# Kernel optimization log

Hardware: AMD Instinct MI355X
Metric: run time of the kernel (lower is better)

The kernel has to match this reference:

```python
import jax, jax.numpy as jnp
import numpy as np


def setup_inputs() -> dict:
    key = jax.random.key(0)
    k1, k2, k3 = jax.random.split(key, 3)
    B, H, S, D = 2, 16, 2048, 64
    return {
        "q": jax.random.normal(k1, (B, H, S, D), dtype=jnp.float32),
        "k": jax.random.normal(k2, (B, H, S, D), dtype=jnp.float32),
        "v": jax.random.normal(k3, (B, H, S, D), dtype=jnp.float32),
        "chunk_size": 256,
    }


def reference(q, k, v, chunk_size):
    # Chunked Based linear attention: linear (K^T V) + rank-3 quadratic (K x K x V)
    # inter-chunk state recurrence (shifted/exclusive cumsum over chunks) plus the
    # intra-chunk causal part with kernel  s = q.k;  phi = s + 0.5*s^2.
    B, H, S, D = q.shape
    C = chunk_size
    N = S // C
    scale = D ** (-0.5)

    qc = (q * scale).reshape(B, H, N, C, D)
    kc = k.reshape(B, H, N, C, D)
    vc = v.reshape(B, H, N, C, D)

    # ---- linear inter-chunk state: shifted cumsum of K^T V per chunk ----
    KV = jnp.einsum("bhncd,bhnce->bhnde", kc, vc)            # (B,H,N,D,D)
    S_lin = jnp.cumsum(KV, axis=2) - KV                       # exclusive cumsum
    o_lin = jnp.einsum("bhncd,bhnde->bhnce", qc, S_lin)

    # ---- quadratic inter-chunk state: shifted cumsum of sum_c K_d K_e V_f ----
    KKV = jnp.einsum("bhncd,bhnce,bhncf->bhndef", kc, kc, vc)  # (B,H,N,D,D,D)
    S_quad = jnp.cumsum(KKV, axis=2) - KKV                     # exclusive cumsum
    o_quad = 0.5 * jnp.einsum("bhndef,bhncd,bhnce->bhncf", S_quad, qc, qc)

    # ---- intra-chunk causal quadratic attention ----
    A = jnp.einsum("bhncd,bhnmd->bhncm", qc, kc)               # (B,H,N,C,C)
    mask = jnp.tril(jnp.ones((C, C), dtype=bool))
    Ak = jnp.where(mask, A + 0.5 * A * A, 0.0)
    o_intra = jnp.einsum("bhncm,bhnmf->bhncf", Ak, vc)

    out = (o_lin + o_quad + o_intra).reshape(B, H, S, D)
    return out
```

## Files before the change

kernel.cpp:

```cpp
#include <hip/hip_runtime.h>
#include <stdint.h>

#define SEQ  2048
#define DH   64
#define BH_N 32
#define SCALE 0.125f

typedef __attribute__((ext_vector_type(8))) short short8;
typedef __attribute__((ext_vector_type(4))) short short4b;
typedef __attribute__((ext_vector_type(4))) float f32x4;

static __device__ __forceinline__ unsigned short f2bf(float f) {
  unsigned int u = __float_as_uint(f);
  u += 0x7fffu + ((u >> 16) & 1u);
  return (unsigned short)(u >> 16);
}
static __device__ __forceinline__ unsigned packbf(float a, float b) {
  unsigned ua = __float_as_uint(a); ua += 0x7fffu + ((ua >> 16) & 1u);
  unsigned ub = __float_as_uint(b); ub += 0x7fffu + ((ub >> 16) & 1u);
  return __builtin_amdgcn_perm(ub, ua, 0x07060302);
}

typedef __attribute__((address_space(1))) const unsigned char* gp1;
typedef __attribute__((address_space(3))) unsigned char* lp3;
static __device__ __forceinline__ void stage16(const void* g, void* l) {
  __builtin_amdgcn_global_load_lds((gp1)g, (lp3)l, 16, 0, 0);
}

__global__ __launch_bounds__(256) void prep_kernel(
    const float* __restrict__ kin, const float* __restrict__ vin,
    unsigned short* __restrict__ kb2, unsigned short* __restrict__ vt2)
{
  const int sb = blockIdx.x;
  const int bh = blockIdx.y;
  const int t  = threadIdx.x;
  __shared__ __align__(16) unsigned short lds[4096];
  const size_t base  = ((size_t)bh * SEQ + (size_t)sb * 64) * DH;
  const size_t obase = ((size_t)bh * 32 + sb) * 4096;

  #pragma unroll
  for (int i = 0; i < 4; ++i) {
    int idx = i * 256 + t, key = idx >> 4, F = (idx & 15) * 4;
    float4 f = *reinterpret_cast<const float4*>(kin + base + key * DH + F);
    int c = (F >> 5) * 4 + ((F >> 3) & 3), jh = (F >> 2) & 1;
    uint2 pk; pk.x = packbf(f.x, f.y); pk.y = packbf(f.z, f.w);
    *reinterpret_cast<uint2*>(lds + (c * 64 + key) * 8 + jh * 4) = pk;
  }
  __syncthreads();
  #pragma unroll
  for (int uu = 0; uu < 2; ++uu) {
    int u = uu * 256 + t;
    *reinterpret_cast<uint4*>(kb2 + obase + u * 8) =
        *reinterpret_cast<const uint4*>(lds + u * 8);
  }
  __syncthreads();
  #pragma unroll
  for (int i = 0; i < 4; ++i) {
    int idx = i * 256 + t, key = idx >> 4, F = (idx & 15) * 4;
    float4 f = *reinterpret_cast<const float4*>(vin + base + key * DH + F);
    int kgp = key >> 5, qd = (key >> 2) & 3, jj = ((key >> 4) & 1) * 4 + (key & 3);
    int u0 = kgp * 256 + (F >> 4) * 64 + qd * 16 + (F & 15);
    lds[(u0 + 0) * 8 + jj] = f2bf(f.x);
    lds[(u0 + 1) * 8 + jj] = f2bf(f.y);
    lds[(u0 + 2) * 8 + jj] = f2bf(f.z);
    lds[(u0 + 3) * 8 + jj] = f2bf(f.w);
  }
  __syncthreads();
  #pragma unroll
  for (int uu = 0; uu < 2; ++uu) {
    int u = uu * 256 + t;
    *reinterpret_cast<uint4*>(vt2 + obase + u * 8) =
        *reinterpret_cast<const uint4*>(lds + u * 8);
  }
}

__global__ __launch_bounds__(256, 2) void attn_kernel(
    const float* __restrict__ q,
    const unsigned short* __restrict__ kb2,
    const unsigned short* __restrict__ vt2,
    float* __restrict__ out)
{
  const int qa   = blockIdx.x;
  const int bh   = blockIdx.y;
  const int tid  = threadIdx.x;
  const int w    = tid >> 6;
  const int lane = tid & 63;
  const int low  = lane & 15;
  const int quad = lane >> 4;
  const int p    = w >> 1;
  const int rh   = w & 1;
  const int nB   = 32 - qa;

  __shared__ __align__(16) unsigned short kls[2][2][4096];
  __shared__ __align__(16) unsigned short vls[2][2][4096];

  const unsigned short* kb_h = kb2 + (size_t)bh * 32 * 4096;
  const unsigned short* v2_h = vt2 + (size_t)bh * 32 * 4096;

  short8 aqA[2][2], aqB[2][2];
  #pragma unroll
  for (int tsel = 0; tsel < 2; ++tsel) {
    const int qt = tsel ? (31 - qa) : qa;
    #pragma unroll
    for (int h = 0; h < 2; ++h) {
      const float* qp =
          q + ((size_t)bh * SEQ + qt * 64 + rh * 32 + h * 16 + low) * DH + quad * 8;
      #pragma unroll
      for (int ks = 0; ks < 2; ++ks) {
        float4 f0 = *reinterpret_cast<const float4*>(qp + ks * 32);
        float4 f1 = *reinterpret_cast<const float4*>(qp + ks * 32 + 4);
        uint4 uv;
        uv.x = packbf(f0.x * SCALE, f0.y * SCALE);
        uv.y = packbf(f0.z * SCALE, f0.w * SCALE);
        uv.z = packbf(f1.x * SCALE, f1.y * SCALE);
        uv.w = packbf(f1.z * SCALE, f1.w * SCALE);
        short8 a = __builtin_bit_cast(short8, uv);
        if (tsel) aqB[h][ks] = a; else aqA[h][ks] = a;
      }
    }
  }

  f32x4 oaccA[2][4], oaccB[2][4];
  #pragma unroll
  for (int h = 0; h < 2; ++h)
    #pragma unroll
    for (int i = 0; i < 4; ++i) {
      oaccA[h][i] = (f32x4){0.f, 0.f, 0.f, 0.f};
      oaccB[h][i] = (f32x4){0.f, 0.f, 0.f, 0.f};
    }

  const int slot = w & 1;
  const unsigned short* gsrc = (w >> 1) ? v2_h : kb_h;
  unsigned short* ldst0 = (w >> 1) ? &vls[0][slot][0] : &kls[0][slot][0];
  unsigned short* ldst1 = (w >> 1) ? &vls[1][slot][0] : &kls[1][slot][0];

  #define STAGE(I, B)                                                          \
    do {                                                                       \
      int s_ = 2 * (I) + slot; if (s_ > 32) s_ = 32;                           \
      const int T_ = (s_ < nB) ? s_ : (s_ - nB);                               \
      const unsigned short* gs_ = gsrc + (size_t)T_ * 4096;                    \
      unsigned short* ld_ = (B) ? ldst1 : ldst0;                               \
      _Pragma("unroll")                                                        \
      for (int r_ = 0; r_ < 8; ++r_)                                           \
        stage16(gs_ + (r_ * 64 + lane) * 8, ld_ + (r_ * 64 + lane) * 8);       \
    } while (0)

  #define COMPUTE(AQ, OACC)                                                    \
    do {                                                                       \
      _Pragma("unroll")                                                        \
      for (int ntp = 0; ntp < 2; ++ntp) {                                      \
        short8 vf[4];                                                          \
        _Pragma("unroll")                                                      \
        for (int ft = 0; ft < 4; ++ft)                                         \
          vf[ft] = *reinterpret_cast<const short8*>(                           \
              vT + ((ntp * 4 + ft) * 64 + quad * 16 + low) * 8);               \
        _Pragma("unroll")                                                      \
        for (int sub = 0; sub < 2; ++sub) {                                    \
          const int nt = ntp * 2 + sub;                                        \
          f32x4 s0 = (f32x4){0.f, 0.f, 0.f, 0.f};                              \
          f32x4 s1 = (f32x4){0.f, 0.f, 0.f, 0.f};                              \
          _Pragma("unroll")                                                    \
          for (int ks = 0; ks < 2; ++ks) {                                     \
            short8 kf = *reinterpret_cast<const short8*>(                      \
                kT + ((ks * 4 + quad) * 64 + nt * 16 + low) * 8);              \
            s0 = __builtin_amdgcn_mfma_f32_16x16x32_bf16(kf, AQ[0][ks], s0, 0, 0, 0); \
            s1 = __builtin_amdgcn_mfma_f32_16x16x32_bf16(kf, AQ[1][ks], s1, 0, 0, 0); \
          }                                                                    \
          _Pragma("unroll")                                                    \
          for (int h = 0; h < 2; ++h) {                                        \
            f32x4 sv = h ? s1 : s0;                                            \
            float pv[4];                                                       \
            _Pragma("unroll")                                                  \
            for (int r = 0; r < 4; ++r) {                                      \
              float x = sv[r];                                                 \
              pv[r] = __builtin_fmaf(0.5f * x, x, x);                          \
            }                                                                  \
            if (diag) {                                                        \
              _Pragma("unroll")                                                \
              for (int r = 0; r < 4; ++r)                                      \
                if ((nt * 16 + quad * 4 + r) > (rh * 32 + h * 16 + low))       \
                  pv[r] = 0.f;                                                 \
            }                                                                  \
            uint2 du; du.x = packbf(pv[0], pv[1]); du.y = packbf(pv[2], pv[3]);\
            short4b pf = __builtin_bit_cast(short4b, du);                      \
            _Pragma("unroll")                                                  \
            for (int ft = 0; ft < 4; ++ft) {                                   \
              short4b va = sub                                                 \
                  ? __builtin_shufflevector(vf[ft], vf[ft], 4, 5, 6, 7)        \
                  : __builtin_shufflevector(vf[ft], vf[ft], 0, 1, 2, 3);       \
              OACC[h][ft] = __builtin_amdgcn_mfma_f32_16x16x16bf16_1k(         \
                  va, pf, OACC[h][ft], 0, 0, 0);                               \
            }                                                                  \
          }                                                                    \
        }                                                                      \
      }                                                                        \
    } while (0)

  STAGE(0, 0);

  for (int i = 0; i < 17; ++i) {
    const int b = i & 1;
    __builtin_amdgcn_s_barrier();
    if (i < 16) {
      STAGE(i + 1, b ^ 1);
      asm volatile("s_waitcnt vmcnt(8)" ::: "memory");
    } else {
      asm volatile("s_waitcnt vmcnt(0)" ::: "memory");
    }
    __builtin_amdgcn_s_barrier();
    asm volatile("" ::: "memory");

    const int s = 2 * i + p;
    if (s > 32) continue;
    const bool diag = (s == nB - 1) || (s == 32);
    const unsigned short* kT = &kls[b][p][0];
    const unsigned short* vT = &vls[b][p][0];

    if (s >= nB) COMPUTE(aqA, oaccA);
    else         COMPUTE(aqB, oaccB);
  }

  __syncthreads();
  float* mb = reinterpret_cast<float*>(&kls[0][0][0]);
  float* mw = mb + rh * 4096;
  if (p == 1) {
    #pragma unroll
    for (int h = 0; h < 2; ++h)
      #pragma unroll
      for (int ft = 0; ft < 4; ++ft) {
        *reinterpret_cast<f32x4*>(mw + ((0 * 8 + h * 4 + ft) * 256 + lane * 4)) =
            oaccA[h][ft];
        *reinterpret_cast<f32x4*>(mw + ((1 * 8 + h * 4 + ft) * 256 + lane * 4)) =
            oaccB[h][ft];
      }
  }
  __syncthreads();
  if (p == 0) {
    #pragma unroll
    for (int tsel = 0; tsel < 2; ++tsel) {
      const int qt = tsel ? (31 - qa) : qa;
      #pragma unroll
      for (int h = 0; h < 2; ++h)
        #pragma unroll
        for (int ft = 0; ft < 4; ++ft) {
          f32x4 o = tsel ? oaccB[h][ft] : oaccA[h][ft];
          f32x4 m = *reinterpret_cast<const f32x4*>(
              mw + ((tsel * 8 + h * 4 + ft) * 256 + lane * 4));
          o += m;
          *reinterpret_cast<f32x4*>(
              out + ((size_t)bh * SEQ + qt * 64 + rh * 32 + h * 16 + low) * DH +
              ft * 16 + quad * 4) = o;
        }
    }
  }
}

extern "C" void kernel_launch(void* const* d_in, const int* in_sizes, int n_in,
                              void* d_out, int out_size, void* d_ws, size_t ws_size,
                              hipStream_t stream)
{
  const float* q = (const float*)d_in[0];
  const float* k = (const float*)d_in[1];
  const float* v = (const float*)d_in[2];
  float* out = (float*)d_out;

  unsigned short* kb2 = (unsigned short*)d_ws;
  unsigned short* vt2 = kb2 + (size_t)BH_N * SEQ * DH;

  prep_kernel<<<dim3(32, BH_N), 256, 0, stream>>>(k, v, kb2, vt2);
  attn_kernel<<<dim3(16, BH_N), 256, 0, stream>>>(q, kb2, vt2, out);
}
```

Before: 129.4 us.

## Use 16x16x32 MFMA for PV product with permuted K/V layouts and hardware bf16 pack

Changes the second matmul (P·V) from two 16x16x16 bf16 MFMAs per 32 keys to one 16x16x32 MFMA. The K row ordering and V transpose layout in the prep kernel are permuted so each lane's score outputs line up with an 8-wide bf16 operand without shuffles. Software round-to-nearest bf16 packing is also replaced by the v_cvt_pk_bf16_f32 instruction. This halves PV MFMA issue count and trims conversion ALU work, at the cost of a more intricate layout and more live score registers.

```diff
diff --git a/kernel.cpp b/kernel.cpp
--- a/kernel.cpp
+++ b/kernel.cpp
@@ -7,7 +7,6 @@
 #define SCALE 0.125f
 
 typedef __attribute__((ext_vector_type(8))) short short8;
-typedef __attribute__((ext_vector_type(4))) short short4b;
 typedef __attribute__((ext_vector_type(4))) float f32x4;
 
 static __device__ __forceinline__ unsigned short f2bf(float f) {
@@ -15,10 +14,10 @@
   u += 0x7fffu + ((u >> 16) & 1u);
   return (unsigned short)(u >> 16);
 }
-static __device__ __forceinline__ unsigned packbf(float a, float b) {
-  unsigned ua = __float_as_uint(a); ua += 0x7fffu + ((ua >> 16) & 1u);
-  unsigned ub = __float_as_uint(b); ub += 0x7fffu + ((ub >> 16) & 1u);
-  return __builtin_amdgcn_perm(ub, ua, 0x07060302);
+static __device__ __forceinline__ unsigned cvtpk(float a, float b) {
+  unsigned r;
+  asm("v_cvt_pk_bf16_f32 %0, %1, %2" : "=v"(r) : "v"(a), "v"(b));
+  return r;
 }
 
 typedef __attribute__((address_space(1))) const unsigned char* gp1;
@@ -42,9 +41,10 @@
   for (int i = 0; i < 4; ++i) {
     int idx = i * 256 + t, key = idx >> 4, F = (idx & 15) * 4;
     float4 f = *reinterpret_cast<const float4*>(kin + base + key * DH + F);
+    int pos = (key & 32) | ((key & 4) << 2) | ((key & 24) >> 1) | (key & 3);
     int c = (F >> 5) * 4 + ((F >> 3) & 3), jh = (F >> 2) & 1;
-    uint2 pk; pk.x = packbf(f.x, f.y); pk.y = packbf(f.z, f.w);
-    *reinterpret_cast<uint2*>(lds + (c * 64 + key) * 8 + jh * 4) = pk;
+    uint2 pk; pk.x = cvtpk(f.x, f.y); pk.y = cvtpk(f.z, f.w);
+    *reinterpret_cast<uint2*>(lds + (c * 64 + pos) * 8 + jh * 4) = pk;
   }
   __syncthreads();
   #pragma unroll
@@ -58,8 +58,8 @@
   for (int i = 0; i < 4; ++i) {
     int idx = i * 256 + t, key = idx >> 4, F = (idx & 15) * 4;
     float4 f = *reinterpret_cast<const float4*>(vin + base + key * DH + F);
-    int kgp = key >> 5, qd = (key >> 2) & 3, jj = ((key >> 4) & 1) * 4 + (key & 3);
-    int u0 = kgp * 256 + (F >> 4) * 64 + qd * 16 + (F & 15);
+    int a = key >> 5, qd = (key >> 3) & 3, jj = key & 7;
+    int u0 = a * 256 + (F >> 4) * 64 + qd * 16 + (F & 15);
     lds[(u0 + 0) * 8 + jj] = f2bf(f.x);
     lds[(u0 + 1) * 8 + jj] = f2bf(f.y);
     lds[(u0 + 2) * 8 + jj] = f2bf(f.z);
@@ -110,10 +110,10 @@
         float4 f0 = *reinterpret_cast<const float4*>(qp + ks * 32);
         float4 f1 = *reinterpret_cast<const float4*>(qp + ks * 32 + 4);
         uint4 uv;
-        uv.x = packbf(f0.x * SCALE, f0.y * SCALE);
-        uv.y = packbf(f0.z * SCALE, f0.w * SCALE);
-        uv.z = packbf(f1.x * SCALE, f1.y * SCALE);
-        uv.w = packbf(f1.z * SCALE, f1.w * SCALE);
+        uv.x = cvtpk(f0.x * SCALE, f0.y * SCALE);
+        uv.y = cvtpk(f0.z * SCALE, f0.w * SCALE);
+        uv.z = cvtpk(f1.x * SCALE, f1.y * SCALE);
+        uv.w = cvtpk(f1.z * SCALE, f1.w * SCALE);
         short8 a = __builtin_bit_cast(short8, uv);
         if (tsel) aqB[h][ks] = a; else aqA[h][ks] = a;
       }
@@ -148,50 +148,52 @@
   #define COMPUTE(AQ, OACC)                                                    \
     do {                                                                       \
       _Pragma("unroll")                                                        \
-      for (int ntp = 0; ntp < 2; ++ntp) {                                      \
-        short8 vf[4];                                                          \
+      for (int a = 0; a < 2; ++a) {                                            \
+        short8 vfa[4];                                                         \
         _Pragma("unroll")                                                      \
         for (int ft = 0; ft < 4; ++ft)                                         \
-          vf[ft] = *reinterpret_cast<const short8*>(                           \
-              vT + ((ntp * 4 + ft) * 64 + quad * 16 + low) * 8);               \
+          vfa[ft] = *reinterpret_cast<const short8*>(                          \
+              vT + ((a * 4 + ft) * 64 + lane) * 8);                            \
+        f32x4 s00 = (f32x4){0.f, 0.f, 0.f, 0.f};                               \
+        f32x4 s01 = s00, s10 = s00, s11 = s00;                                 \
         _Pragma("unroll")                                                      \
-        for (int sub = 0; sub < 2; ++sub) {                                    \
-          const int nt = ntp * 2 + sub;                                        \
-          f32x4 s0 = (f32x4){0.f, 0.f, 0.f, 0.f};                              \
-          f32x4 s1 = (f32x4){0.f, 0.f, 0.f, 0.f};                              \
+        for (int ks = 0; ks < 2; ++ks) {                                       \
+          short8 kf0 = *reinterpret_cast<const short8*>(                       \
+              kT + ((ks * 4 + quad) * 64 + (a * 2 + 0) * 16 + low) * 8);       \
+          short8 kf1 = *reinterpret_cast<const short8*>(                       \
+              kT + ((ks * 4 + quad) * 64 + (a * 2 + 1) * 16 + low) * 8);       \
+          s00 = __builtin_amdgcn_mfma_f32_16x16x32_bf16(kf0, AQ[0][ks], s00, 0, 0, 0); \
+          s01 = __builtin_amdgcn_mfma_f32_16x16x32_bf16(kf0, AQ[1][ks], s01, 0, 0, 0); \
+          s10 = __builtin_amdgcn_mfma_f32_16x16x32_bf16(kf1, AQ[0][ks], s10, 0, 0, 0); \
+          s11 = __builtin_amdgcn_mfma_f32_16x16x32_bf16(kf1, AQ[1][ks], s11, 0, 0, 0); \
+        }                                                                      \
+        _Pragma("unroll")                                                      \
+        for (int h = 0; h < 2; ++h) {                                          \
+          f32x4 sA = h ? s01 : s00;           \
+          f32x4 sB = h ? s11 : s10;           \
+          float pv[8];                                                         \
           _Pragma("unroll")                                                    \
-          for (int ks = 0; ks < 2; ++ks) {                                     \
-            short8 kf = *reinterpret_cast<const short8*>(                      \
-                kT + ((ks * 4 + quad) * 64 + nt * 16 + low) * 8);              \
-            s0 = __builtin_amdgcn_mfma_f32_16x16x32_bf16(kf, AQ[0][ks], s0, 0, 0, 0); \
-            s1 = __builtin_amdgcn_mfma_f32_16x16x32_bf16(kf, AQ[1][ks], s1, 0, 0, 0); \
+          for (int r = 0; r < 4; ++r) {                                        \
+            float x0 = sA[r], x1 = sB[r];                                      \
+            pv[r]     = __builtin_fmaf(0.5f * x0, x0, x0);                     \
+            pv[4 + r] = __builtin_fmaf(0.5f * x1, x1, x1);                     \
           }                                                                    \
-          _Pragma("unroll")                                                    \
-          for (int h = 0; h < 2; ++h) {                                        \
-            f32x4 sv = h ? s1 : s0;                                            \
-            float pv[4];                                                       \
+          if (diag) {                                                          \
+            const int qrow = rh * 32 + h * 16 + low;                           \
             _Pragma("unroll")                                                  \
             for (int r = 0; r < 4; ++r) {                                      \
-              float x = sv[r];                                                 \
-              pv[r] = __builtin_fmaf(0.5f * x, x, x);                          \
-            }                                                                  \
-            if (diag) {                                                        \
-              _Pragma("unroll")                                                \
-              for (int r = 0; r < 4; ++r)                                      \
-                if ((nt * 16 + quad * 4 + r) > (rh * 32 + h * 16 + low))       \
-                  pv[r] = 0.f;                                                 \
-            }                                                                  \
-            uint2 du; du.x = packbf(pv[0], pv[1]); du.y = packbf(pv[2], pv[3]);\
-            short4b pf = __builtin_bit_cast(short4b, du);                      \
-            _Pragma("unroll")                                                  \
-            for (int ft = 0; ft < 4; ++ft) {                                   \
-              short4b va = sub                                                 \
-                  ? __builtin_shufflevector(vf[ft], vf[ft], 4, 5, 6, 7)        \
-                  : __builtin_shufflevector(vf[ft], vf[ft], 0, 1, 2, 3);       \
-              OACC[h][ft] = __builtin_amdgcn_mfma_f32_16x16x16bf16_1k(         \
-                  va, pf, OACC[h][ft], 0, 0, 0);                               \
+              if ((a * 32 + quad * 8 + r) > qrow)     pv[r]     = 0.f;         \
+              if ((a * 32 + quad * 8 + 4 + r) > qrow) pv[4 + r] = 0.f;         \
             }                                                                  \
           }                                                                    \
+          uint4 uu;                                                            \
+          uu.x = cvtpk(pv[0], pv[1]); uu.y = cvtpk(pv[2], pv[3]);              \
+          uu.z = cvtpk(pv[4], pv[5]); uu.w = cvtpk(pv[6], pv[7]);              \
+          short8 pf = __builtin_bit_cast(short8, uu);                          \
+          _Pragma("unroll")                                                    \
+          for (int ft = 0; ft < 4; ++ft)                                       \
+            OACC[h][ft] = __builtin_amdgcn_mfma_f32_16x16x32_bf16(             \
+                vfa[ft], pf, OACC[h][ft], 0, 0, 0);                            \
         }                                                                      \
       }                                                                        \
     } while (0)
```

New measurement: 125.5 us. -3.0%, faster.
